# Kernel tuning notes

Measured on AMD Instinct MI355X. Metric: run time of the kernel, lower is better.

The kernel has to match this reference:

```python
import jax, jax.numpy as jnp
import numpy as np

N_STATIONS = 100000
N_TIME = 1000
K_NEIGH = 8
SMOOTH = 0.2  # smoothing_factor


def setup_inputs() -> dict:
    key = jax.random.key(0)
    ks = jax.random.split(key, 7)
    time_vector = jax.random.uniform(ks[0], (N_TIME,), dtype=jnp.float32) * 5.0
    constant_offset = jax.random.normal(ks[1], (N_STATIONS,), dtype=jnp.float32)
    linear_trend = jax.random.normal(ks[2], (N_STATIONS,), dtype=jnp.float32)
    seasonal_amplitudes = jax.random.uniform(ks[3], (N_STATIONS, 4), dtype=jnp.float32) * 3.0
    seasonal_phases = jax.random.uniform(ks[4], (N_STATIONS, 4), dtype=jnp.float32) * (2.0 * np.pi)
    neighbor_indices = jax.random.randint(ks[5], (N_STATIONS, K_NEIGH), 0, N_STATIONS, dtype=jnp.int32)
    w = jax.random.uniform(ks[6], (N_STATIONS, K_NEIGH), dtype=jnp.float32) + 1e-3
    neighbor_weights = w / jnp.sum(w, axis=1, keepdims=True)  # row-normalized like the kNN weights
    periods = jnp.array([0.25, 0.5, 1.0, 2.0], dtype=jnp.float32)
    return {
        "time_vector": time_vector,
        "constant_offset": constant_offset,
        "linear_trend": linear_trend,
        "seasonal_amplitudes": seasonal_amplitudes,
        "seasonal_phases": seasonal_phases,
        "neighbor_indices": neighbor_indices,
        "neighbor_weights": neighbor_weights,
        "periods": periods,
    }


def _smooth_amp(amps, nbr_idx, nbr_w):
    # amps: [N,4], nbr_idx: [N,K], nbr_w: [N,K]
    nb = amps[nbr_idx]  # [N,K,4]
    avg = jnp.einsum('nkc,nk->nc', nb, nbr_w)
    return (1.0 - SMOOTH) * amps + SMOOTH * avg


def _smooth_phase(phases, nbr_idx, nbr_w):
    # circular-mean smoothing via unit complex vectors, done with real math
    nb = phases[nbr_idx]  # [N,K,4]
    avg_re = jnp.einsum('nkc,nk->nc', jnp.cos(nb), nbr_w)
    avg_im = jnp.einsum('nkc,nk->nc', jnp.sin(nb), nbr_w)
    mix_re = (1.0 - SMOOTH) * jnp.cos(phases) + SMOOTH * avg_re
    mix_im = (1.0 - SMOOTH) * jnp.sin(phases) + SMOOTH * avg_im
    return jnp.arctan2(mix_im, mix_re)


def reference(time_vector, constant_offset, linear_trend, seasonal_amplitudes,
              seasonal_phases, neighbor_indices, neighbor_weights, periods):
    amp_s = _smooth_amp(seasonal_amplitudes, neighbor_indices, neighbor_weights)   # [N,4]
    ph_s = _smooth_phase(seasonal_phases, neighbor_indices, neighbor_weights)      # [N,4]
    t = time_vector[None, :]  # [1,T]
    signals = constant_offset[:, None] + linear_trend[:, None] * t  # [N,T]
    two_pi = jnp.float32(2.0 * np.pi)
    for i in range(4):  # fixed small number of seasonal components
        freq = 1.0 / periods[i]
        signals = signals + amp_s[:, i:i+1] * jnp.sin(two_pi * freq * t + ph_s[:, i:i+1])
    return signals
```

## Files before the change

### kernel.cpp

```cpp
#include <hip/hip_runtime.h>
#include <math.h>

#define N_STATIONS 100000
#define N_TIME     1000
#define K_NEIGH    8
#define SPB        50

#define TTAB_PLANE   N_TIME
#define REC_OFF      8192
#define REC_STRIDE   16

__global__ __launch_bounds__(256) void ttab_kernel(
    const float* __restrict__ time_vector,
    const float* __restrict__ periods,
    float*       __restrict__ ws)
{
    const int tid = threadIdx.x;
    if (tid >= 250) return;
    const float TWO_PI = 6.28318530717958647692f;
    const float4 tv = *(const float4*)(time_vector + 4 * tid);
    float t4[4] = { tv.x, tv.y, tv.z, tv.w };
#pragma unroll
    for (int i = 0; i < 4; ++i) {
        const float w = TWO_PI / periods[i];
        float4 s4, c4;
        float* sp = &s4.x;
        float* cp = &c4.x;
#pragma unroll
        for (int j = 0; j < 4; ++j) sincosf(w * t4[j], &sp[j], &cp[j]);
        *(float4*)(ws + (2 * i)     * TTAB_PLANE + 4 * tid) = s4;
        *(float4*)(ws + (2 * i + 1) * TTAB_PLANE + 4 * tid) = c4;
    }
}

__global__ __launch_bounds__(256) void coef_kernel(
    const float* __restrict__ constant_offset,
    const float* __restrict__ linear_trend,
    const float* __restrict__ amps,
    const float* __restrict__ phases,
    const int*   __restrict__ nbr_idx,
    const float* __restrict__ nbr_w,
    float*       __restrict__ ws)
{
    const int g = blockIdx.x * 256 + threadIdx.x;
    if (g >= N_STATIONS * 4) return;
    const int n = g >> 2;
    const int c = g & 3;

    const float a0 = amps[g];
    const float p0 = phases[g];

    float accA = 0.f, accRe = 0.f, accIm = 0.f;
#pragma unroll
    for (int k = 0; k < K_NEIGH; ++k) {
        const int   idx = nbr_idx[n * 8 + k];
        const float w   = nbr_w[n * 8 + k];
        const float a   = amps[idx * 4 + c];
        const float p   = phases[idx * 4 + c];
        float sp, cp;
        sincosf(p, &sp, &cp);
        accA  = fmaf(w, a,  accA);
        accRe = fmaf(w, cp, accRe);
        accIm = fmaf(w, sp, accIm);
    }
    const float amp_s = 0.8f * a0 + 0.2f * accA;
    float s0, c0;
    sincosf(p0, &s0, &c0);
    const float mre = 0.8f * c0 + 0.2f * accRe;
    const float mim = 0.8f * s0 + 0.2f * accIm;
    const float r2  = mre * mre + mim * mim;
    float cs, cc;
    if (r2 > 1e-30f) {
        const float rinv = rsqrtf(r2);
        cs = amp_s * mre * rinv;
        cc = amp_s * mim * rinv;
    } else {
        cs = amp_s;
        cc = 0.f;
    }
    float* rec = ws + REC_OFF + (size_t)n * REC_STRIDE;
    rec[c]     = cs;
    rec[4 + c] = cc;
    if (c == 0) {
        rec[8] = constant_offset[n];
        rec[9] = linear_trend[n];
    }
}

__global__ __launch_bounds__(256) void insar_main(
    const float* __restrict__ time_vector,
    const float* __restrict__ ws,
    float*       __restrict__ out)
{
    const int tid = threadIdx.x;
    if (tid >= 250) return;
    const int n0 = blockIdx.x * SPB;

    const float4 tv = *(const float4*)(time_vector + 4 * tid);
    float t4[4] = { tv.x, tv.y, tv.z, tv.w };

    float st[4][4], ct[4][4];
#pragma unroll
    for (int i = 0; i < 4; ++i) {
        const float4 s4 = *(const float4*)(ws + (2 * i)     * TTAB_PLANE + 4 * tid);
        const float4 c4 = *(const float4*)(ws + (2 * i + 1) * TTAB_PLANE + 4 * tid);
        st[i][0] = s4.x; st[i][1] = s4.y; st[i][2] = s4.z; st[i][3] = s4.w;
        ct[i][0] = c4.x; ct[i][1] = c4.y; ct[i][2] = c4.z; ct[i][3] = c4.w;
    }

    const float* rec0 = ws + REC_OFF + (size_t)n0 * REC_STRIDE;
    float* orow = out + (size_t)n0 * N_TIME + 4 * tid;

    for (int s = 0; s < SPB; ++s) {
        const float* rec = rec0 + s * REC_STRIDE;
        const float cs0 = rec[0], cs1 = rec[1], cs2 = rec[2], cs3 = rec[3];
        const float cc0 = rec[4], cc1 = rec[5], cc2 = rec[6], cc3 = rec[7];
        const float off = rec[8], tr = rec[9];

        float4 o;
        float* op = &o.x;
#pragma unroll
        for (int j = 0; j < 4; ++j) {
            float v = fmaf(tr, t4[j], off);
            v = fmaf(cs0, st[0][j], v);
            v = fmaf(cc0, ct[0][j], v);
            v = fmaf(cs1, st[1][j], v);
            v = fmaf(cc1, ct[1][j], v);
            v = fmaf(cs2, st[2][j], v);
            v = fmaf(cc2, ct[2][j], v);
            v = fmaf(cs3, st[3][j], v);
            v = fmaf(cc3, ct[3][j], v);
            op[j] = v;
        }
        *(float4*)orow = o;
        orow += N_TIME;
    }
}

extern "C" void kernel_launch(void* const* d_in, const int* in_sizes, int n_in,
                              void* d_out, int out_size, void* d_ws, size_t ws_size,
                              hipStream_t stream) {
    const float* time_vector     = (const float*)d_in[0];
    const float* constant_offset = (const float*)d_in[1];
    const float* linear_trend    = (const float*)d_in[2];
    const float* amps            = (const float*)d_in[3];
    const float* phases          = (const float*)d_in[4];
    const int*   nbr_idx         = (const int*)  d_in[5];
    const float* nbr_w           = (const float*)d_in[6];
    const float* periods         = (const float*)d_in[7];
    float* out = (float*)d_out;
    float* ws  = (float*)d_ws;

    ttab_kernel<<<1, 256, 0, stream>>>(time_vector, periods, ws);
    const int coef_blocks = (N_STATIONS * 4 + 255) / 256;
    coef_kernel<<<coef_blocks, 256, 0, stream>>>(constant_offset, linear_trend,
                                                 amps, phases, nbr_idx, nbr_w, ws);
    insar_main<<<N_STATIONS / SPB, 256, 0, stream>>>(time_vector, ws, out);
}
```

Before: 451.6 us.

## Merge table and coefficient kernels, vectorize per-station gathers, prefetch records

Folds the time-table kernel into the coefficient kernel as an extra block, which removes one launch. The coefficient kernel now runs one thread per station instead of one per station-component, gathering each neighbour's four amplitudes and phases as float4 and writing the record with vector stores. The main kernel prefetches the next station's record one iteration ahead and adds a launch_bounds occupancy hint. The prep kernel has a quarter as many threads, each doing more sincos work, and that costs parallelism. The main kernel is dominated by the 400MB of output writes, so it is unlikely to change much.

```diff
diff --git a/kernel.cpp b/kernel.cpp
--- a/kernel.cpp
+++ b/kernel.cpp
@@ -9,31 +9,11 @@
 #define TTAB_PLANE   N_TIME
 #define REC_OFF      8192
 #define REC_STRIDE   16
+#define COEF_BLOCKS  391
 
-__global__ __launch_bounds__(256) void ttab_kernel(
+__global__ __launch_bounds__(256) void prep_kernel(
     const float* __restrict__ time_vector,
     const float* __restrict__ periods,
-    float*       __restrict__ ws)
-{
-    const int tid = threadIdx.x;
-    if (tid >= 250) return;
-    const float TWO_PI = 6.28318530717958647692f;
-    const float4 tv = *(const float4*)(time_vector + 4 * tid);
-    float t4[4] = { tv.x, tv.y, tv.z, tv.w };
-#pragma unroll
-    for (int i = 0; i < 4; ++i) {
-        const float w = TWO_PI / periods[i];
-        float4 s4, c4;
-        float* sp = &s4.x;
-        float* cp = &c4.x;
-#pragma unroll
-        for (int j = 0; j < 4; ++j) sincosf(w * t4[j], &sp[j], &cp[j]);
-        *(float4*)(ws + (2 * i)     * TTAB_PLANE + 4 * tid) = s4;
-        *(float4*)(ws + (2 * i + 1) * TTAB_PLANE + 4 * tid) = c4;
-    }
-}
-
-__global__ __launch_bounds__(256) void coef_kernel(
     const float* __restrict__ constant_offset,
     const float* __restrict__ linear_trend,
     const float* __restrict__ amps,
@@ -42,52 +22,92 @@
     const float* __restrict__ nbr_w,
     float*       __restrict__ ws)
 {
-    const int g = blockIdx.x * 256 + threadIdx.x;
-    if (g >= N_STATIONS * 4) return;
-    const int n = g >> 2;
-    const int c = g & 3;
+    const int tid = threadIdx.x;
 
-    const float a0 = amps[g];
-    const float p0 = phases[g];
+    if (blockIdx.x == COEF_BLOCKS) {
+        if (tid >= 250) return;
+        const float TWO_PI = 6.28318530717958647692f;
+        const float4 tv = *(const float4*)(time_vector + 4 * tid);
+        float t4[4] = { tv.x, tv.y, tv.z, tv.w };
+#pragma unroll
+        for (int i = 0; i < 4; ++i) {
+            const float w = TWO_PI / periods[i];
+            float4 s4, c4;
+            float* sp = &s4.x;
+            float* cp = &c4.x;
+#pragma unroll
+            for (int j = 0; j < 4; ++j) sincosf(w * t4[j], &sp[j], &cp[j]);
+            *(float4*)(ws + (2 * i)     * TTAB_PLANE + 4 * tid) = s4;
+            *(float4*)(ws + (2 * i + 1) * TTAB_PLANE + 4 * tid) = c4;
+        }
+        return;
+    }
 
-    float accA = 0.f, accRe = 0.f, accIm = 0.f;
+    const int n = blockIdx.x * 256 + tid;
+    if (n >= N_STATIONS) return;
+
+    const int4   i0 = *(const int4*)  (nbr_idx + n * 8);
+    const int4   i1 = *(const int4*)  (nbr_idx + n * 8 + 4);
+    const float4 w0 = *(const float4*)(nbr_w   + n * 8);
+    const float4 w1 = *(const float4*)(nbr_w   + n * 8 + 4);
+    const float4 a_own = *(const float4*)(amps   + n * 4);
+    const float4 p_own = *(const float4*)(phases + n * 4);
+
+    const int   idxs[8] = { i0.x, i0.y, i0.z, i0.w, i1.x, i1.y, i1.z, i1.w };
+    const float wts[8]  = { w0.x, w0.y, w0.z, w0.w, w1.x, w1.y, w1.z, w1.w };
+
+    float accA[4]  = {0.f, 0.f, 0.f, 0.f};
+    float accRe[4] = {0.f, 0.f, 0.f, 0.f};
+    float accIm[4] = {0.f, 0.f, 0.f, 0.f};
 #pragma unroll
     for (int k = 0; k < K_NEIGH; ++k) {
-        const int   idx = nbr_idx[n * 8 + k];
-        const float w   = nbr_w[n * 8 + k];
-        const float a   = amps[idx * 4 + c];
-        const float p   = phases[idx * 4 + c];
-        float sp, cp;
-        sincosf(p, &sp, &cp);
-        accA  = fmaf(w, a,  accA);
-        accRe = fmaf(w, cp, accRe);
-        accIm = fmaf(w, sp, accIm);
+        const int   idx = idxs[k];
+        const float w   = wts[k];
+        const float4 a = *(const float4*)(amps   + idx * 4);
+        const float4 p = *(const float4*)(phases + idx * 4);
+        const float* ap = &a.x;
+        const float* pp = &p.x;
+#pragma unroll
+        for (int c = 0; c < 4; ++c) {
+            float sp, cp;
+            sincosf(pp[c], &sp, &cp);
+            accA[c]  = fmaf(w, ap[c], accA[c]);
+            accRe[c] = fmaf(w, cp,    accRe[c]);
+            accIm[c] = fmaf(w, sp,    accIm[c]);
+        }
     }
-    const float amp_s = 0.8f * a0 + 0.2f * accA;
-    float s0, c0;
-    sincosf(p0, &s0, &c0);
-    const float mre = 0.8f * c0 + 0.2f * accRe;
-    const float mim = 0.8f * s0 + 0.2f * accIm;
-    const float r2  = mre * mre + mim * mim;
-    float cs, cc;
-    if (r2 > 1e-30f) {
-        const float rinv = rsqrtf(r2);
-        cs = amp_s * mre * rinv;
-        cc = amp_s * mim * rinv;
-    } else {
-        cs = amp_s;
-        cc = 0.f;
+
+    float4 csv, ccv;
+    float* csp = &csv.x;
+    float* ccp = &ccv.x;
+    const float* aop = &a_own.x;
+    const float* pop = &p_own.x;
+#pragma unroll
+    for (int c = 0; c < 4; ++c) {
+        const float amp_s = 0.8f * aop[c] + 0.2f * accA[c];
+        float s0, c0;
+        sincosf(pop[c], &s0, &c0);
+        const float mre = 0.8f * c0 + 0.2f * accRe[c];
+        const float mim = 0.8f * s0 + 0.2f * accIm[c];
+        const float r2  = mre * mre + mim * mim;
+        if (r2 > 1e-30f) {
+            const float rinv = rsqrtf(r2);
+            csp[c] = amp_s * mre * rinv;
+            ccp[c] = amp_s * mim * rinv;
+        } else {
+            csp[c] = amp_s;
+            ccp[c] = 0.f;
+        }
     }
+
     float* rec = ws + REC_OFF + (size_t)n * REC_STRIDE;
-    rec[c]     = cs;
-    rec[4 + c] = cc;
-    if (c == 0) {
-        rec[8] = constant_offset[n];
-        rec[9] = linear_trend[n];
-    }
+    *(float4*)(rec)     = csv;
+    *(float4*)(rec + 4) = ccv;
+    rec[8] = constant_offset[n];
+    rec[9] = linear_trend[n];
 }
 
-__global__ __launch_bounds__(256) void insar_main(
+__global__ __launch_bounds__(256, 8) void insar_main(
     const float* __restrict__ time_vector,
     const float* __restrict__ ws,
     float*       __restrict__ out)
@@ -111,29 +131,37 @@
     const float* rec0 = ws + REC_OFF + (size_t)n0 * REC_STRIDE;
     float* orow = out + (size_t)n0 * N_TIME + 4 * tid;
 
+    float r[10];
+#pragma unroll
+    for (int q = 0; q < 10; ++q) r[q] = rec0[q];
+
     for (int s = 0; s < SPB; ++s) {
-        const float* rec = rec0 + s * REC_STRIDE;
-        const float cs0 = rec[0], cs1 = rec[1], cs2 = rec[2], cs3 = rec[3];
-        const float cc0 = rec[4], cc1 = rec[5], cc2 = rec[6], cc3 = rec[7];
-        const float off = rec[8], tr = rec[9];
+        const int sn = (s + 1 < SPB) ? (s + 1) : (SPB - 1);
+        const float* recn = rec0 + sn * REC_STRIDE;
+        float rn[10];
+#pragma unroll
+        for (int q = 0; q < 10; ++q) rn[q] = recn[q];
 
         float4 o;
         float* op = &o.x;
 #pragma unroll
         for (int j = 0; j < 4; ++j) {
-            float v = fmaf(tr, t4[j], off);
-            v = fmaf(cs0, st[0][j], v);
-            v = fmaf(cc0, ct[0][j], v);
-            v = fmaf(cs1, st[1][j], v);
-            v = fmaf(cc1, ct[1][j], v);
-            v = fmaf(cs2, st[2][j], v);
-            v = fmaf(cc2, ct[2][j], v);
-            v = fmaf(cs3, st[3][j], v);
-            v = fmaf(cc3, ct[3][j], v);
+            float v = fmaf(r[9], t4[j], r[8]);
+            v = fmaf(r[0], st[0][j], v);
+            v = fmaf(r[4], ct[0][j], v);
+            v = fmaf(r[1], st[1][j], v);
+            v = fmaf(r[5], ct[1][j], v);
+            v = fmaf(r[2], st[2][j], v);
+            v = fmaf(r[6], ct[2][j], v);
+            v = fmaf(r[3], st[3][j], v);
+            v = fmaf(r[7], ct[3][j], v);
             op[j] = v;
         }
         *(float4*)orow = o;
         orow += N_TIME;
+
+#pragma unroll
+        for (int q = 0; q < 10; ++q) r[q] = rn[q];
     }
 }
 
@@ -151,9 +179,9 @@
     float* out = (float*)d_out;
     float* ws  = (float*)d_ws;
 
-    ttab_kernel<<<1, 256, 0, stream>>>(time_vector, periods, ws);
-    const int coef_blocks = (N_STATIONS * 4 + 255) / 256;
-    coef_kernel<<<coef_blocks, 256, 0, stream>>>(constant_offset, linear_trend,
-                                                 amps, phases, nbr_idx, nbr_w, ws);
+    prep_kernel<<<COEF_BLOCKS + 1, 256, 0, stream>>>(
+        time_vector, periods, constant_offset, linear_trend,
+        amps, phases, nbr_idx, nbr_w, ws);
+
     insar_main<<<N_STATIONS / SPB, 256, 0, stream>>>(time_vector, ws, out);
 }
```

After: 449.3 us. About the same (-0.5%).
